# Performance work log

Measured on AMD Instinct MI355X. Metric: run time of the kernel, lower is better.

The kernel has to match this reference:

```python
import jax, jax.numpy as jnp
import numpy as np

N_SPECIES = 4; N_BASIS = 128; N_GRAPH = 16; R_MAX = 6.0
NS_NODE, NV_NODE = 32, 16          # node irreps 32x0e + 16x1o
NS_EDGE = 16                       # initial edge irreps 16x0e
NS_OUT, NV_OUT = 16, 8             # output irreps 16x0e + 8x1o
NS_IN = 2 * NS_NODE + NS_EDGE      # 80 concatenated scalars
NV_IN = 2 * NV_NODE                # 32 concatenated vectors
NS_CONV = NS_OUT + NV_OUT          # 24 scalars (16 features + 8 gates)
W_SIZES = [NS_IN * NS_CONV, NS_IN * NV_OUT, NV_IN * NV_OUT, NV_IN * NS_CONV, NV_IN * NV_OUT]
N_NODES, N_EDGES = 8192, 65536
EPS = 1e-5


def gaussian_basis(d, stop, n):
    offsets = jnp.linspace(0.0, stop, n)
    coeff = -0.5 / (offsets[1] - offsets[0]) ** 2
    return jnp.exp(coeff * (d[:, None] - offsets[None, :]) ** 2)


def seg_mean(vals, seg, cnt):
    return jax.ops.segment_sum(vals, seg, num_segments=N_GRAPH) / cnt[:, None]


def setup_inputs():
    key = jax.random.key(0)
    ks = jax.random.split(key, 20)
    rn = lambda k, shape, scale: jax.random.normal(k, shape, jnp.float32) * scale
    inp = {}
    inp["node_fea"] = rn(ks[0], (N_NODES, NS_NODE + 3 * NV_NODE), 1.0)
    d = 0.5 + 5.0 * jax.random.uniform(ks[1], (N_EDGES,), jnp.float32)
    vec = jax.random.normal(ks[2], (N_EDGES, 3), jnp.float32)
    inp["edge_attr"] = jnp.concatenate([d[:, None], vec], axis=1)
    inp["edge_index"] = jax.random.randint(ks[3], (2, N_EDGES), 0, N_NODES)
    inp["x"] = jax.random.randint(ks[4], (N_NODES,), 0, N_SPECIES)
    inp["batch"] = jnp.sort(jax.random.randint(ks[5], (N_NODES,), 0, N_GRAPH))
    inp["w_rh"] = rn(ks[6], (N_BASIS, 64), N_BASIS ** -0.5); inp["b_rh"] = jnp.zeros((64,), jnp.float32)
    inp["w_ro"] = rn(ks[7], (64, sum(W_SIZES)), 64 ** -0.5); inp["b_ro"] = jnp.zeros((sum(W_SIZES),), jnp.float32)
    inp["w_pre"] = rn(ks[8], (NS_EDGE, NS_EDGE), NS_EDGE ** -0.5); inp["b_pre"] = jnp.zeros((NS_EDGE,), jnp.float32)
    inp["w_sc"] = rn(ks[9], (NS_EDGE, N_SPECIES ** 2, NS_OUT), 1.0)
    inp["w_post_s"] = rn(ks[10], (NS_OUT, NS_OUT), NS_OUT ** -0.5); inp["b_post_s"] = jnp.zeros((NS_OUT,), jnp.float32)
    inp["w_post_v"] = rn(ks[11], (NV_OUT, NV_OUT), NV_OUT ** -0.5)
    inp["ln_w_s"] = jnp.ones((NS_OUT,), jnp.float32); inp["ln_b_s"] = jnp.zeros((NS_OUT,), jnp.float32)
    inp["ln_w_v"] = jnp.ones((NV_OUT,), jnp.float32)
    inp["w_skip"] = rn(ks[12], (NS_EDGE, NS_OUT), NS_EDGE ** -0.5)
    inp["w_edge_s"] = rn(ks[13], (NS_OUT, NS_OUT), NS_OUT ** -0.5); inp["b_edge_s"] = jnp.zeros((NS_OUT,), jnp.float32)
    inp["w_edge_v"] = rn(ks[14], (NV_OUT, NV_OUT), NV_OUT ** -0.5)
    return inp


def _forward(node_fea, edge_attr, w_rh, b_rh, w_ro, b_ro, w_pre, b_pre, w_sc,
             w_post_s, b_post_s, w_post_v, ln_w_s, ln_b_s, ln_w_v,
             w_skip, w_edge_s, b_edge_s, w_edge_v, edge_index, x, batch):
    E = edge_index.shape[1]
    idx_i, idx_j = edge_index[0], edge_index[1]
    one_hot = jax.nn.one_hot(N_SPECIES * x[idx_i] + x[idx_j], N_SPECIES ** 2, dtype=node_fea.dtype)
    d, vec = edge_attr[:, 0], edge_attr[:, 1:4]
    u = vec / (jnp.linalg.norm(vec, axis=1, keepdims=True) + 1e-12)
    Y1 = np.sqrt(3.0) * u                                   # l=1 sph harm, component norm; Y0 == 1
    rbf = gaussian_basis(d, R_MAX, N_BASIS)                 # edge_length_embedded
    edge_s0 = gaussian_basis(d, 6.0, NS_EDGE)               # distance_expansion -> initial edge scalars
    # self connection: edge scalars x species-pair one-hot -> output scalars
    sc = jnp.einsum('ei,ej,ijo->eo', edge_s0, one_hot, w_sc) / np.sqrt(NS_EDGE * N_SPECIES ** 2)
    edge_s = edge_s0 @ w_pre + b_pre                        # lin_pre
    # gather node features by edge indices and concat
    nf_i, nf_j = node_fea[idx_i], node_fea[idx_j]
    s_in = jnp.concatenate([nf_i[:, :NS_NODE], nf_j[:, :NS_NODE], edge_s], axis=1)  # [E,80]
    v_in = jnp.concatenate([nf_i[:, NS_NODE:].reshape(E, NV_NODE, 3),
                            nf_j[:, NS_NODE:].reshape(E, NV_NODE, 3)], axis=1)      # [E,32,3]
    # radial MLP -> per-edge tensor-product path weights
    h = jax.nn.silu(rbf @ w_rh + b_rh)
    w_all = h @ w_ro + b_ro                                 # [E, 3840]
    w1, w2, w3, w4, w5 = jnp.split(w_all, np.cumsum(W_SIZES)[:-1].tolist(), axis=1)
    # equivariant tensor-product paths (explicit l<=1 Clebsch-Gordan structure)
    s0 = jnp.einsum('ei,eio->eo', s_in, w1.reshape(E, NS_IN, NS_CONV)) / np.sqrt(NS_IN)            # 0e x 0e -> 0e
    vA = jnp.einsum('ei,eio,ec->eoc', s_in, w2.reshape(E, NS_IN, NV_OUT), Y1) / np.sqrt(NS_IN)     # 0e x 1o -> 1o
    vB = jnp.einsum('eic,eio->eoc', v_in, w3.reshape(E, NV_IN, NV_OUT)) / np.sqrt(NV_IN)           # 1o x 0e -> 1o
    s1 = jnp.einsum('eic,eio,ec->eo', v_in, w4.reshape(E, NV_IN, NS_CONV), Y1) / np.sqrt(3.0 * NV_IN)  # 1o.1o -> 0e
    vC = jnp.einsum('eic,eio->eoc', jnp.cross(v_in, Y1[:, None, :]), w5.reshape(E, NV_IN, NV_OUT)) / np.sqrt(2.0 * NV_IN)  # 1o x 1o -> 1o
    s_conv = s0 + s1                                        # [E,24]
    v_conv = vA + vB + vC                                   # [E,8,3]
    # gate nonlinearity inside conv
    s_out = jax.nn.silu(s_conv[:, :NS_OUT])
    v_out = v_conv * jax.nn.sigmoid(s_conv[:, NS_OUT:])[:, :, None]
    # lin_post then self connection
    s_out = s_out @ w_post_s + b_post_s + sc
    v_out = jnp.einsum('eic,io->eoc', v_out, w_post_v)
    # e3LayerNorm keyed by graph id of source node
    eb = batch[idx_i]
    cnt = jnp.maximum(jax.ops.segment_sum(jnp.ones((E,), s_out.dtype), eb, num_segments=N_GRAPH), 1.0)
    mu = seg_mean(s_out, eb, cnt)
    s_c = s_out - mu[eb]
    rms_s = jnp.sqrt(seg_mean(s_c ** 2, eb, cnt).mean(axis=1, keepdims=True) + EPS)
    s_n = s_c / rms_s[eb] * ln_w_s + ln_b_s
    rms_v = jnp.sqrt((seg_mean((v_out ** 2).sum(-1), eb, cnt) / 3.0).mean(axis=1, keepdims=True) + EPS)
    v_n = v_out / rms_v[eb][:, :, None] * ln_w_v[None, :, None]
    # skip connection from old edge features (scalars only)
    s_n = s_n + edge_s0 @ w_skip
    # final lin_edge
    s_fin = s_n @ w_edge_s + b_edge_s
    v_fin = jnp.einsum('eic,io->eoc', v_n, w_edge_v)
    return jnp.concatenate([s_fin, v_fin.reshape(E, NV_OUT * 3)], axis=1)  # [E,40]


def reference(node_fea, edge_attr, edge_index, x, batch, w_rh, b_rh, w_ro, b_ro,
              w_pre, b_pre, w_sc, w_post_s, b_post_s, w_post_v, ln_w_s, ln_b_s, ln_w_v,
              w_skip, w_edge_s, b_edge_s, w_edge_v):
    return _forward(node_fea, edge_attr, w_rh, b_rh, w_ro, b_ro, w_pre, b_pre, w_sc,
                    w_post_s, b_post_s, w_post_v, ln_w_s, ln_b_s, ln_w_v,
                    w_skip, w_edge_s, b_edge_s, w_edge_v, edge_index, x, batch)
```

## Files before the change

kernel.cpp:

```cpp
#include <hip/hip_runtime.h>

typedef unsigned short u16;
typedef unsigned int u32;
typedef __attribute__((ext_vector_type(8))) short short8;
typedef __attribute__((ext_vector_type(4))) float floatx4;

#define E_TOTAL 65536

__device__ __forceinline__ u16 f2bf(float f) {
    union { float f; u32 i; } c; c.f = f;
    const u32 u = c.i;
    const u32 r = (u + 0x7fffu + ((u >> 16) & 1u)) >> 16;
    return (u16)r;
}
__device__ __forceinline__ float bfu2f(u16 u) {
    union { u32 i; float f; } c; c.i = ((u32)u) << 16; return c.f;
}
__device__ __forceinline__ void split2(float x0, float x1, u32& hp, u32& lp) {
    union { float f; u32 u; } a0, a1, h0, h1, l0, l1;
    a0.f = x0; a1.f = x1;
    h0.u = a0.u & 0xFFFF0000u; h1.u = a1.u & 0xFFFF0000u;
    hp = __builtin_amdgcn_perm(a1.u, a0.u, 0x07060302u);
    l0.f = x0 - h0.f; l1.f = x1 - h1.f;
    lp = __builtin_amdgcn_perm(l1.u, l0.u, 0x07060302u);
}
union Frag8 { u32 u[4]; short8 s; };


__global__ __launch_bounds__(64) void k_init(float* __restrict__ ws, int* __restrict__ binv) {
    const int lane = threadIdx.x;
    for (int i = lane; i < 1056; i += 64) ws[i] = 0.0f;
    const int q = lane >> 4;
    if (lane < 32) binv[lane] = lane;
    short8 bfr;
    #pragma unroll
    for (int j = 0; j < 8; ++j) bfr[j] = (short)f2bf((float)(q*8 + j + 1));
    #pragma unroll
    for (int s = 0; s < 32; ++s) {
        const int qa = s >> 3, ja = s & 7;
        short8 afr = {0,0,0,0,0,0,0,0};
        if (q == qa) afr[ja] = (short)f2bf(1.0f);
        floatx4 dc = {0.0f, 0.0f, 0.0f, 0.0f};
        dc = __builtin_amdgcn_mfma_f32_16x16x32_bf16(afr, bfr, dc, 0, 0, 0);
        if (lane == 0) {
            const int sB = (int)(dc[0] + 0.5f) - 1;
            if (sB >= 0 && sB < 32) binv[sB] = s;
        }
    }
}

__global__ __launch_bounds__(256) void k_edge_heavy(
    const float* __restrict__ node_fea, const float* __restrict__ edge_attr,
    const int* __restrict__ edge_index, const int* __restrict__ xsp,
    const float* __restrict__ w_rh, const float* __restrict__ b_rh,
    const float* __restrict__ w_ro, const float* __restrict__ b_ro,
    const float* __restrict__ w_pre, const float* __restrict__ b_pre,
    const float* __restrict__ w_sc, const float* __restrict__ w_post_s,
    const float* __restrict__ b_post_s, const float* __restrict__ w_post_v,
    const int* __restrict__ binv,
    float* __restrict__ out)
{
    __shared__ __align__(16) char pool[32 * 129 * 4];
    __shared__ float sh_sin[32][81];
    __shared__ float sh_vl[32][3][32];
    __shared__ float sh_acc[32][56];
    __shared__ float sh_es0[32][16];
    __shared__ float sh_y1[32][4];
    __shared__ int   sh_kmap[32];

    u16* pool16 = (u16*)pool;
    float (*sh_wt)[129] = (float(*)[129])pool;

    const int tid = threadIdx.x;
    const int ed = tid >> 4, l16 = tid & 15;
    const int lane = tid & 63, w = tid >> 6;
    const int quad = lane >> 4, l15 = lane & 15;

    if (tid < 32) sh_kmap[tid] = binv[tid];

    const float C128 = -0.5f * (127.0f/6.0f) * (127.0f/6.0f);
    const float S128 = 6.0f/127.0f;
    const float rs80 = 0.11180339887498949f;
    const float rs32 = 0.17677669529663689f;

    int pp[2];
    #pragma unroll
    for (int g = 0; g < 2; ++g) {
        const int e  = blockIdx.x * 32 + g*16 + ed;
        const int ge = g*16 + ed;
        const int ni = edge_index[e];
        const int nj = edge_index[E_TOTAL + e];
        pp[g] = 4*xsp[ni] + xsp[nj];
        const float4 ea = *(const float4*)(edge_attr + 4*e);
        const float d  = ea.x;
        const float vx = ea.y, vy = ea.z, vz = ea.w;
        const float invn = 1.0f / (sqrtf(vx*vx + vy*vy + vz*vz) + 1e-12f);
        if (l16 == 0) {
            sh_y1[ge][0] = 1.7320508075688772f * vx * invn;
            sh_y1[ge][1] = 1.7320508075688772f * vy * invn;
            sh_y1[ge][2] = 1.7320508075688772f * vz * invn;
        }
        {
            short8 thi, tlo;
            #pragma unroll
            for (int r = 0; r < 8; ++r) {
                const int b = l16*8 + r;
                const float t = d - S128 * (float)b;
                const float x = expf(C128 * t * t);
                const u16 hi = f2bf(x);
                thi[r] = (short)hi;
                tlo[r] = (short)f2bf(x - bfu2f(hi));
            }
            *(short8*)&pool16[(0*2 + g)*2048 + (l16*16 + ed)*8] = thi;
            *(short8*)&pool16[(1*2 + g)*2048 + (l16*16 + ed)*8] = tlo;
        }
        {
            const float t = d - 0.4f * (float)l16;
            sh_es0[ge][l16] = expf(-3.125f * t * t);
        }
        {
            const float* fi = node_fea + (size_t)ni * 80;
            const float* fj = node_fea + (size_t)nj * 80;
            sh_sin[ge][2*l16+0]    = fi[2*l16+0] * rs80;
            sh_sin[ge][2*l16+1]    = fi[2*l16+1] * rs80;
            sh_sin[ge][32+2*l16+0] = fj[2*l16+0] * rs80;
            sh_sin[ge][32+2*l16+1] = fj[2*l16+1] * rs80;
            #pragma unroll
            for (int c = 0; c < 3; ++c) {
                sh_vl[ge][c][l16]      = fi[32 + 3*l16 + c] * rs32;
                sh_vl[ge][c][16 + l16] = fj[32 + 3*l16 + c] * rs32;
            }
        }
    }
    for (int s = tid; s < 32*56; s += 256) (&sh_acc[0][0])[s] = 0.0f;
    __syncthreads();

    int km[8];
    u32 voff0[8], voff1[8];
    #pragma unroll
    for (int j = 0; j < 8; ++j) {
        km[j] = sh_kmap[quad*8 + j];
        voff0[j] = (u32)(km[j] * 3840 + l15);
        voff1[j] = voff0[j] + 32u * 3840u;
    }

    float my_sc[2];
    #pragma unroll
    for (int g = 0; g < 2; ++g) {
        const int ge = g*16 + ed;
        const int o = l16;
        float es = b_pre[o];
        float sc = 0.0f;
        const int p = pp[g];
        #pragma unroll
        for (int i = 0; i < 16; ++i) {
            const float gg = sh_es0[ge][i];
            es += gg * w_pre[i*16 + o];
            sc += gg * w_sc[(i*16 + p)*16 + o];
        }
        sh_sin[ge][64 + o] = es * rs80;
        my_sc[g] = sc * 0.0625f;
    }

    floatx4 hacc[2] = {{0,0,0,0},{0,0,0,0}};
    #pragma unroll
    for (int kk = 0; kk < 4; ++kk) {
        Frag8 bh, bl;
        #pragma unroll
        for (int jj = 0; jj < 4; ++jj) {
            const float x0 = w_rh[(size_t)(kk*32 + km[2*jj+0])*64 + w*16 + l15];
            const float x1 = w_rh[(size_t)(kk*32 + km[2*jj+1])*64 + w*16 + l15];
            split2(x0, x1, bh.u[jj], bl.u[jj]);
        }
        #pragma unroll
        for (int g = 0; g < 2; ++g) {
            const short8 ahi = *(const short8*)&pool16[(0*2 + g)*2048 + ((kk*4 + quad)*16 + l15)*8];
            const short8 alo = *(const short8*)&pool16[(1*2 + g)*2048 + ((kk*4 + quad)*16 + l15)*8];
            hacc[g] = __builtin_amdgcn_mfma_f32_16x16x32_bf16(ahi, bh.s, hacc[g], 0, 0, 0);
            hacc[g] = __builtin_amdgcn_mfma_f32_16x16x32_bf16(alo, bh.s, hacc[g], 0, 0, 0);
            hacc[g] = __builtin_amdgcn_mfma_f32_16x16x32_bf16(ahi, bl.s, hacc[g], 0, 0, 0);
        }
    }
    __syncthreads();
    {
        const int hn = w*16 + l15;
        const float bb = b_rh[hn];
        const int k8 = hn >> 3, j2 = hn & 7;
        #pragma unroll
        for (int g = 0; g < 2; ++g) {
            #pragma unroll
            for (int r = 0; r < 4; ++r) {
                const float x = hacc[g][r] + bb;
                const float s = x / (1.0f + expf(-x));
                const int m = quad*4 + r;
                const u16 h = f2bf(s);
                pool16[(0*2 + g)*1024 + (k8*16 + m)*8 + j2] = h;
                pool16[(1*2 + g)*1024 + (k8*16 + m)*8 + j2] = f2bf(s - bfu2f(h));
            }
        }
    }
    __syncthreads();
    short8 ah_[2][2], al_[2][2];
    #pragma unroll
    for (int f = 0; f < 2; ++f)
        #pragma unroll
        for (int g = 0; g < 2; ++g) {
            ah_[f][g] = *(const short8*)&pool16[(0*2 + g)*1024 + ((f*4 + quad)*16 + l15)*8];
            al_[f][g] = *(const short8*)&pool16[(1*2 + g)*1024 + ((f*4 + quad)*16 + l15)*8];
        }

    for (int ch = 0; ch < 30; ++ch) {
        const int coff = ch * 128;
        floatx4 acc[2][2];
        float bias[2];
        #pragma unroll
        for (int ct = 0; ct < 2; ++ct) {
            const int sgct = __builtin_amdgcn_readfirstlane(ch*8 + w*2 + ct);
            const float* bp = w_ro + sgct*16;
            float f0[8], f1[8];
            #pragma unroll
            for (int j = 0; j < 8; ++j) {
                f0[j] = bp[voff0[j]];
                f1[j] = bp[voff1[j]];
            }
            Frag8 b0h, b0l, b1h, b1l;
            #pragma unroll
            for (int jj = 0; jj < 4; ++jj) {
                split2(f0[2*jj], f0[2*jj+1], b0h.u[jj], b0l.u[jj]);
                split2(f1[2*jj], f1[2*jj+1], b1h.u[jj], b1l.u[jj]);
            }
            #pragma unroll
            for (int g = 0; g < 2; ++g) {
                floatx4 a = {0.0f, 0.0f, 0.0f, 0.0f};
                a = __builtin_amdgcn_mfma_f32_16x16x32_bf16(ah_[0][g], b0h.s, a, 0, 0, 0);
                a = __builtin_amdgcn_mfma_f32_16x16x32_bf16(ah_[1][g], b1h.s, a, 0, 0, 0);
                a = __builtin_amdgcn_mfma_f32_16x16x32_bf16(al_[0][g], b0h.s, a, 0, 0, 0);
                a = __builtin_amdgcn_mfma_f32_16x16x32_bf16(al_[1][g], b1h.s, a, 0, 0, 0);
                a = __builtin_amdgcn_mfma_f32_16x16x32_bf16(ah_[0][g], b0l.s, a, 0, 0, 0);
                a = __builtin_amdgcn_mfma_f32_16x16x32_bf16(ah_[1][g], b1l.s, a, 0, 0, 0);
                acc[ct][g] = a;
            }
            bias[ct] = b_ro[sgct*16 + l15];
        }
        __syncthreads();
        #pragma unroll
        for (int ct = 0; ct < 2; ++ct) {
            const int col = w*32 + ct*16 + l15;
            #pragma unroll
            for (int g = 0; g < 2; ++g)
                #pragma unroll
                for (int r = 0; r < 4; ++r)
                    sh_wt[g*16 + quad*4 + r][col] = acc[ct][g][r] + bias[ct];
        }
        __syncthreads();

        if (ch < 15) {
            for (int idx = tid; idx < 768; idx += 256) {
                const int eo = idx / 24, o = idx % 24;
                const int i0 = (coff > o) ? (coff - o + 23) / 24 : 0;
                int i1 = (coff + 128 - o + 23) / 24; if (i1 > 80) i1 = 80;
                float a = 0.0f;
                for (int i = i0; i < i1; ++i)
                    a += sh_sin[eo][i] * sh_wt[eo][i*24 + o - coff];
                sh_acc[eo][o] += a;
            }
        } else if (ch < 20) {
            const int ib = (ch - 15) * 16;
            const int eo = tid >> 3, o = tid & 7;
            float a = 0.0f;
            #pragma unroll
            for (int i = 0; i < 16; ++i)
                a += sh_sin[eo][ib + i] * sh_wt[eo][i*8 + o];
            sh_acc[eo][24 + o] += a;
        } else if (ch < 22) {
            const int ib = (ch - 20) * 16;
            for (int idx = tid; idx < 768; idx += 256) {
                const int eo = idx / 24, rem = idx % 24;
                const int o = rem / 3, cc = rem % 3;
                float a = 0.0f;
                #pragma unroll
                for (int i = 0; i < 16; ++i)
                    a += sh_vl[eo][cc][ib + i] * sh_wt[eo][i*8 + o];
                sh_acc[eo][32 + o*3 + cc] += a;
            }
        } else if (ch < 28) {
            const int rel = coff - 2816;
            for (int idx = tid; idx < 768; idx += 256) {
                const int eo = idx / 24, o = idx % 24;
                const int i0 = (rel > o) ? (rel - o + 23) / 24 : 0;
                int i1 = (rel + 128 - o + 23) / 24; if (i1 > 32) i1 = 32;
                float t0 = 0.0f, t1 = 0.0f, t2 = 0.0f;
                for (int i = i0; i < i1; ++i) {
                    const float wv = sh_wt[eo][i*24 + o - rel];
                    t0 += sh_vl[eo][0][i] * wv;
                    t1 += sh_vl[eo][1][i] * wv;
                    t2 += sh_vl[eo][2][i] * wv;
                }
                sh_acc[eo][o] += (t0*sh_y1[eo][0] + t1*sh_y1[eo][1] + t2*sh_y1[eo][2])
                                 * 0.57735026918962573f;
            }
        } else {
            const int ib = (ch - 28) * 16;
            const int eo = tid >> 3, o = tid & 7;
            float t0 = 0.0f, t1 = 0.0f, t2 = 0.0f;
            #pragma unroll
            for (int i = 0; i < 16; ++i) {
                const float wv = sh_wt[eo][i*8 + o];
                t0 += sh_vl[eo][0][ib + i] * wv;
                t1 += sh_vl[eo][1][ib + i] * wv;
                t2 += sh_vl[eo][2][ib + i] * wv;
            }
            const float Ya = sh_y1[eo][0], Yb = sh_y1[eo][1], Yc = sh_y1[eo][2];
            sh_acc[eo][32 + o*3 + 0] += 0.70710678118654746f * (t1*Yc - t2*Yb);
            sh_acc[eo][32 + o*3 + 1] += 0.70710678118654746f * (t2*Ya - t0*Yc);
            sh_acc[eo][32 + o*3 + 2] += 0.70710678118654746f * (t0*Yb - t1*Ya);
        }
    }
    __syncthreads();

    #pragma unroll
    for (int g = 0; g < 2; ++g) {
        const int e  = blockIdx.x * 32 + g*16 + ed;
        const int ge = g*16 + ed;
        {
            const int o = l16;
            float a = b_post_s[o] + my_sc[g];
            #pragma unroll
            for (int i = 0; i < 16; ++i) {
                const float sv = sh_acc[ge][i];
                a += (sv / (1.0f + expf(-sv))) * w_post_s[i*16 + o];
            }
            out[(size_t)e*40 + o] = a;
        }
        if (l16 < 8) {
            const int o = l16;
            const float Ya = sh_y1[ge][0], Yb = sh_y1[ge][1], Yc = sh_y1[ge][2];
            float r0 = 0.0f, r1 = 0.0f, r2 = 0.0f;
            #pragma unroll
            for (int i = 0; i < 8; ++i) {
                const float gg = 1.0f / (1.0f + expf(-sh_acc[ge][16 + i]));
                const float a2 = sh_acc[ge][24 + i];
                const float ww = w_post_v[i*8 + o];
                r0 += (a2*Ya + sh_acc[ge][32 + i*3 + 0]) * gg * ww;
                r1 += (a2*Yb + sh_acc[ge][32 + i*3 + 1]) * gg * ww;
                r2 += (a2*Yc + sh_acc[ge][32 + i*3 + 2]) * gg * ww;
            }
            out[(size_t)e*40 + 16 + o*3 + 0] = r0;
            out[(size_t)e*40 + 16 + o*3 + 1] = r1;
            out[(size_t)e*40 + 16 + o*3 + 2] = r2;
        }
    }
}

__global__ __launch_bounds__(256) void k_stats_partial(
    const float* __restrict__ sv, const int* __restrict__ edge_index,
    const int* __restrict__ batch, float* __restrict__ ws)
{
    __shared__ float sh_ed[256][41];
    __shared__ int   sh_eb[256];
    const int tid = threadIdx.x;
    const int e = blockIdx.x * 256 + tid;
    sh_eb[tid] = batch[edge_index[e]];
    const float* p = sv + (size_t)e * 40;
    #pragma unroll
    for (int j = 0; j < 40; ++j) sh_ed[tid][j] = p[j];
    __syncthreads();

    for (int slot = tid; slot < 768; slot += 256) {
        const int g = slot / 48, s = slot % 48;
        float acc = 0.0f;
        if (s < 16) {
            for (int k = 0; k < 256; ++k) {
                const float m = (sh_eb[k] == g) ? 1.0f : 0.0f;
                acc += m * sh_ed[k][s];
            }
        } else if (s < 32) {
            for (int k = 0; k < 256; ++k) {
                const float m = (sh_eb[k] == g) ? 1.0f : 0.0f;
                const float v = sh_ed[k][s - 16];
                acc += m * v * v;
            }
        } else if (s < 40) {
            const int o3 = 16 + (s - 32) * 3;
            for (int k = 0; k < 256; ++k) {
                const float m = (sh_eb[k] == g) ? 1.0f : 0.0f;
                const float v0 = sh_ed[k][o3], v1 = sh_ed[k][o3+1], v2 = sh_ed[k][o3+2];
                acc += m * (v0*v0 + v1*v1 + v2*v2);
            }
        } else if (s == 40) {
            for (int k = 0; k < 256; ++k) acc += (sh_eb[k] == g) ? 1.0f : 0.0f;
        }
        atomicAdd(&ws[slot], acc);
    }
}

__global__ __launch_bounds__(64) void k_stats_final(float* __restrict__ ws)
{
    const int tid = threadIdx.x;
    if (tid < 16) {
        const int g = tid;
        float cnt = ws[g*48 + 40]; if (cnt < 1.0f) cnt = 1.0f;
        const float ic = 1.0f / cnt;
        float vs = 0.0f;
        for (int chn = 0; chn < 16; ++chn) {
            const float mu = ws[g*48 + chn] * ic;
            ws[768 + g*16 + chn] = mu;
            vs += ws[g*48 + 16 + chn] * ic - mu * mu;
        }
        if (vs < 0.0f) vs = 0.0f;
        ws[1024 + g] = 1.0f / sqrtf(vs * (1.0f/16.0f) + 1e-5f);
        float vv = 0.0f;
        for (int o = 0; o < 8; ++o) vv += ws[g*48 + 32 + o];
        vv = vv * ic * (1.0f/3.0f) * (1.0f/8.0f);
        ws[1040 + g] = 1.0f / sqrtf(vv + 1e-5f);
    }
}

__global__ __launch_bounds__(256) void k_edge_final(
    float* buf, const float* __restrict__ ws,
    const float* __restrict__ edge_attr, const int* __restrict__ edge_index,
    const int* __restrict__ batch,
    const float* __restrict__ ln_w_s, const float* __restrict__ ln_b_s,
    const float* __restrict__ ln_w_v, const float* __restrict__ w_skip,
    const float* __restrict__ w_edge_s, const float* __restrict__ b_edge_s,
    const float* __restrict__ w_edge_v)
{
    __shared__ float sh_mu[16][16];
    __shared__ float sh_is[16], sh_iv[16];
    __shared__ float sh_lws[16], sh_lbs[16], sh_lwv[8];
    __shared__ float sh_skip[16][16], sh_wes[16][16], sh_bes[16], sh_wev[8][8];
    const int tid = threadIdx.x;
    sh_mu[tid >> 4][tid & 15]   = ws[768 + tid];
    sh_skip[tid >> 4][tid & 15] = w_skip[tid];
    sh_wes[tid >> 4][tid & 15]  = w_edge_s[tid];
    if (tid < 16) {
        sh_is[tid]  = ws[1024 + tid];
        sh_iv[tid]  = ws[1040 + tid];
        sh_lws[tid] = ln_w_s[tid];
        sh_lbs[tid] = ln_b_s[tid];
        sh_bes[tid] = b_edge_s[tid];
    }
    if (tid < 8)  sh_lwv[tid] = ln_w_v[tid];
    if (tid < 64) sh_wev[tid >> 3][tid & 7] = w_edge_v[tid];
    __syncthreads();

    const int e = blockIdx.x * 256 + tid;
    const int g = batch[edge_index[e]];
    const float d = edge_attr[4*e];
    float es0[16];
    #pragma unroll
    for (int b = 0; b < 16; ++b) {
        const float t = d - 0.4f * (float)b;
        es0[b] = expf(-3.125f * t * t);
    }
    float p[40];
    float* pb = buf + (size_t)e * 40;
    #pragma unroll
    for (int j = 0; j < 40; ++j) p[j] = pb[j];

    const float is = sh_is[g];
    float sn[16];
    #pragma unroll
    for (int chn = 0; chn < 16; ++chn)
        sn[chn] = (p[chn] - sh_mu[g][chn]) * is * sh_lws[chn] + sh_lbs[chn];
    #pragma unroll
    for (int b = 0; b < 16; ++b) {
        const float g0 = es0[b];
        #pragma unroll
        for (int chn = 0; chn < 16; ++chn) sn[chn] += g0 * sh_skip[b][chn];
    }
    #pragma unroll
    for (int o = 0; o < 16; ++o) {
        float a = sh_bes[o];
        #pragma unroll
        for (int chn = 0; chn < 16; ++chn) a += sn[chn] * sh_wes[chn][o];
        pb[o] = a;
    }
    const float iv = sh_iv[g];
    float vn[8][3];
    #pragma unroll
    for (int i = 0; i < 8; ++i) {
        const float f = iv * sh_lwv[i];
        vn[i][0] = p[16 + i*3 + 0] * f;
        vn[i][1] = p[16 + i*3 + 1] * f;
        vn[i][2] = p[16 + i*3 + 2] * f;
    }
    #pragma unroll
    for (int o = 0; o < 8; ++o) {
        float r0 = 0.0f, r1 = 0.0f, r2 = 0.0f;
        #pragma unroll
        for (int i = 0; i < 8; ++i) {
            const float w = sh_wev[i][o];
            r0 += vn[i][0] * w; r1 += vn[i][1] * w; r2 += vn[i][2] * w;
        }
        pb[16 + o*3 + 0] = r0;
        pb[16 + o*3 + 1] = r1;
        pb[16 + o*3 + 2] = r2;
    }
}

extern "C" void kernel_launch(void* const* d_in, const int* in_sizes, int n_in,
                              void* d_out, int out_size, void* d_ws, size_t ws_size,
                              hipStream_t stream)
{
    const float* node_fea  = (const float*)d_in[0];
    const float* edge_attr = (const float*)d_in[1];
    const int* edge_index  = (const int*)d_in[2];
    const int* xsp         = (const int*)d_in[3];
    const int* batch       = (const int*)d_in[4];
    const float* w_rh      = (const float*)d_in[5];
    const float* b_rh      = (const float*)d_in[6];
    const float* w_ro      = (const float*)d_in[7];
    const float* b_ro      = (const float*)d_in[8];
    const float* w_pre     = (const float*)d_in[9];
    const float* b_pre     = (const float*)d_in[10];
    const float* w_sc      = (const float*)d_in[11];
    const float* w_post_s  = (const float*)d_in[12];
    const float* b_post_s  = (const float*)d_in[13];
    const float* w_post_v  = (const float*)d_in[14];
    const float* ln_w_s    = (const float*)d_in[15];
    const float* ln_b_s    = (const float*)d_in[16];
    const float* ln_w_v    = (const float*)d_in[17];
    const float* w_skip    = (const float*)d_in[18];
    const float* w_edge_s  = (const float*)d_in[19];
    const float* b_edge_s  = (const float*)d_in[20];
    const float* w_edge_v  = (const float*)d_in[21];

    float* ws   = (float*)d_ws;
    int*   binv = (int*)(ws + 1056);
    float* out  = (float*)d_out;

    k_init<<<1, 64, 0, stream>>>(ws, binv);
    k_edge_heavy<<<2048, 256, 0, stream>>>(node_fea, edge_attr, edge_index, xsp,
        w_rh, b_rh, w_ro, b_ro, w_pre, b_pre, w_sc, w_post_s, b_post_s, w_post_v,
        binv, out);
    k_stats_partial<<<256, 256, 0, stream>>>(out, edge_index, batch, ws);
    k_stats_final<<<1, 64, 0, stream>>>(ws);
    k_edge_final<<<256, 256, 0, stream>>>(out, ws, edge_attr, edge_index,
        batch, ln_w_s, ln_b_s, ln_w_v, w_skip, w_edge_s, b_edge_s, w_edge_v);
}
```

Before: 491.2 us.

## Fuse graph stats into edge kernel, prefetch weights, keep accumulators in registers

Moves the per-graph statistics reduction into the heavy edge kernel, which removes the k_stats_partial pass that re-read the whole output. Atomics now use 64-bit fixed-point integers, which makes the sums deterministic. The w_ro fragment loads are software-pipelined one chunk ahead. Per-edge accumulators move from shared memory into registers, and launch bounds request 3 blocks per SM. In exchange, the kernel issues far more global atomics (2048 blocks instead of 256), register pressure goes up, and the fixed-point scale could overflow or lose precision.

```diff
diff --git a/kernel.cpp b/kernel.cpp
--- a/kernel.cpp
+++ b/kernel.cpp
@@ -2,10 +2,13 @@
 
 typedef unsigned short u16;
 typedef unsigned int u32;
+typedef unsigned long long u64;
 typedef __attribute__((ext_vector_type(8))) short short8;
 typedef __attribute__((ext_vector_type(4))) float floatx4;
 
 #define E_TOTAL 65536
+#define STAT_SCALE 67108864.0f
+#define STAT_INV   (1.0 / 67108864.0)
 
 __device__ __forceinline__ u16 f2bf(float f) {
     union { float f; u32 i; } c; c.f = f;
@@ -29,7 +32,7 @@
 
 __global__ __launch_bounds__(64) void k_init(float* __restrict__ ws, int* __restrict__ binv) {
     const int lane = threadIdx.x;
-    for (int i = lane; i < 1056; i += 64) ws[i] = 0.0f;
+    for (int i = lane; i < 1824; i += 64) ws[i] = 0.0f;
     const int q = lane >> 4;
     if (lane < 32) binv[lane] = lane;
     short8 bfr;
@@ -49,7 +52,7 @@
     }
 }
 
-__global__ __launch_bounds__(256) void k_edge_heavy(
+__global__ __launch_bounds__(256, 3) void k_edge_heavy(
     const float* __restrict__ node_fea, const float* __restrict__ edge_attr,
     const int* __restrict__ edge_index, const int* __restrict__ xsp,
     const float* __restrict__ w_rh, const float* __restrict__ b_rh,
@@ -57,8 +60,8 @@
     const float* __restrict__ w_pre, const float* __restrict__ b_pre,
     const float* __restrict__ w_sc, const float* __restrict__ w_post_s,
     const float* __restrict__ b_post_s, const float* __restrict__ w_post_v,
-    const int* __restrict__ binv,
-    float* __restrict__ out)
+    const int* __restrict__ binv, const int* __restrict__ batch,
+    float* __restrict__ out, float* __restrict__ ws)
 {
     __shared__ __align__(16) char pool[32 * 129 * 4];
     __shared__ float sh_sin[32][81];
@@ -67,9 +70,11 @@
     __shared__ float sh_es0[32][16];
     __shared__ float sh_y1[32][4];
     __shared__ int   sh_kmap[32];
+    __shared__ int   sh_eb[32];
 
     u16* pool16 = (u16*)pool;
     float (*sh_wt)[129] = (float(*)[129])pool;
+    float* psf = (float*)pool;
 
     const int tid = threadIdx.x;
     const int ed = tid >> 4, l16 = tid & 15;
@@ -99,6 +104,7 @@
             sh_y1[ge][0] = 1.7320508075688772f * vx * invn;
             sh_y1[ge][1] = 1.7320508075688772f * vy * invn;
             sh_y1[ge][2] = 1.7320508075688772f * vz * invn;
+            sh_eb[ge] = batch[ni];
         }
         {
             short8 thi, tlo;
@@ -132,7 +138,6 @@
             }
         }
     }
-    for (int s = tid; s < 32*56; s += 256) (&sh_acc[0][0])[s] = 0.0f;
     __syncthreads();
 
     int km[8];
@@ -209,25 +214,37 @@
             al_[f][g] = *(const short8*)&pool16[(1*2 + g)*1024 + ((f*4 + quad)*16 + l15)*8];
         }
 
+    float rs[3] = {0.0f, 0.0f, 0.0f};
+    float ra2   = 0.0f;
+    float rv[3] = {0.0f, 0.0f, 0.0f};
+
+    float fB[32];
+    float biasv[2];
+    {
+        #pragma unroll
+        for (int ct = 0; ct < 2; ++ct) {
+            const int sgct = __builtin_amdgcn_readfirstlane(w*2 + ct);
+            const float* bp = w_ro + sgct*16;
+            #pragma unroll
+            for (int j = 0; j < 8; ++j) {
+                fB[ct*16 + j]     = bp[voff0[j]];
+                fB[ct*16 + 8 + j] = bp[voff1[j]];
+            }
+            biasv[ct] = b_ro[sgct*16 + l15];
+        }
+    }
+
     for (int ch = 0; ch < 30; ++ch) {
         const int coff = ch * 128;
         floatx4 acc[2][2];
-        float bias[2];
+        float biasc[2] = {biasv[0], biasv[1]};
         #pragma unroll
         for (int ct = 0; ct < 2; ++ct) {
-            const int sgct = __builtin_amdgcn_readfirstlane(ch*8 + w*2 + ct);
-            const float* bp = w_ro + sgct*16;
-            float f0[8], f1[8];
-            #pragma unroll
-            for (int j = 0; j < 8; ++j) {
-                f0[j] = bp[voff0[j]];
-                f1[j] = bp[voff1[j]];
-            }
             Frag8 b0h, b0l, b1h, b1l;
             #pragma unroll
             for (int jj = 0; jj < 4; ++jj) {
-                split2(f0[2*jj], f0[2*jj+1], b0h.u[jj], b0l.u[jj]);
-                split2(f1[2*jj], f1[2*jj+1], b1h.u[jj], b1l.u[jj]);
+                split2(fB[ct*16 + 2*jj],     fB[ct*16 + 2*jj + 1],     b0h.u[jj], b0l.u[jj]);
+                split2(fB[ct*16 + 8 + 2*jj], fB[ct*16 + 8 + 2*jj + 1], b1h.u[jj], b1l.u[jj]);
             }
             #pragma unroll
             for (int g = 0; g < 2; ++g) {
@@ -240,7 +257,19 @@
                 a = __builtin_amdgcn_mfma_f32_16x16x32_bf16(ah_[1][g], b1l.s, a, 0, 0, 0);
                 acc[ct][g] = a;
             }
-            bias[ct] = b_ro[sgct*16 + l15];
+        }
+        if (ch + 1 < 30) {
+            #pragma unroll
+            for (int ct = 0; ct < 2; ++ct) {
+                const int sgct = __builtin_amdgcn_readfirstlane((ch+1)*8 + w*2 + ct);
+                const float* bp = w_ro + sgct*16;
+                #pragma unroll
+                for (int j = 0; j < 8; ++j) {
+                    fB[ct*16 + j]     = bp[voff0[j]];
+                    fB[ct*16 + 8 + j] = bp[voff1[j]];
+                }
+                biasv[ct] = b_ro[sgct*16 + l15];
+            }
         }
         __syncthreads();
         #pragma unroll
@@ -250,19 +279,21 @@
             for (int g = 0; g < 2; ++g)
                 #pragma unroll
                 for (int r = 0; r < 4; ++r)
-                    sh_wt[g*16 + quad*4 + r][col] = acc[ct][g][r] + bias[ct];
+                    sh_wt[g*16 + quad*4 + r][col] = acc[ct][g][r] + biasc[ct];
         }
         __syncthreads();
 
         if (ch < 15) {
-            for (int idx = tid; idx < 768; idx += 256) {
+            #pragma unroll
+            for (int t3 = 0; t3 < 3; ++t3) {
+                const int idx = tid + 256*t3;
                 const int eo = idx / 24, o = idx % 24;
                 const int i0 = (coff > o) ? (coff - o + 23) / 24 : 0;
                 int i1 = (coff + 128 - o + 23) / 24; if (i1 > 80) i1 = 80;
                 float a = 0.0f;
                 for (int i = i0; i < i1; ++i)
                     a += sh_sin[eo][i] * sh_wt[eo][i*24 + o - coff];
-                sh_acc[eo][o] += a;
+                rs[t3] += a;
             }
         } else if (ch < 20) {
             const int ib = (ch - 15) * 16;
@@ -271,21 +302,25 @@
             #pragma unroll
             for (int i = 0; i < 16; ++i)
                 a += sh_sin[eo][ib + i] * sh_wt[eo][i*8 + o];
-            sh_acc[eo][24 + o] += a;
+            ra2 += a;
         } else if (ch < 22) {
             const int ib = (ch - 20) * 16;
-            for (int idx = tid; idx < 768; idx += 256) {
+            #pragma unroll
+            for (int t3 = 0; t3 < 3; ++t3) {
+                const int idx = tid + 256*t3;
                 const int eo = idx / 24, rem = idx % 24;
                 const int o = rem / 3, cc = rem % 3;
                 float a = 0.0f;
                 #pragma unroll
                 for (int i = 0; i < 16; ++i)
                     a += sh_vl[eo][cc][ib + i] * sh_wt[eo][i*8 + o];
-                sh_acc[eo][32 + o*3 + cc] += a;
+                rv[t3] += a;
             }
         } else if (ch < 28) {
             const int rel = coff - 2816;
-            for (int idx = tid; idx < 768; idx += 256) {
+            #pragma unroll
+            for (int t3 = 0; t3 < 3; ++t3) {
+                const int idx = tid + 256*t3;
                 const int eo = idx / 24, o = idx % 24;
                 const int i0 = (rel > o) ? (rel - o + 23) / 24 : 0;
                 int i1 = (rel + 128 - o + 23) / 24; if (i1 > 32) i1 = 32;
@@ -296,25 +331,40 @@
                     t1 += sh_vl[eo][1][i] * wv;
                     t2 += sh_vl[eo][2][i] * wv;
                 }
-                sh_acc[eo][o] += (t0*sh_y1[eo][0] + t1*sh_y1[eo][1] + t2*sh_y1[eo][2])
-                                 * 0.57735026918962573f;
+                rs[t3] += (t0*sh_y1[eo][0] + t1*sh_y1[eo][1] + t2*sh_y1[eo][2])
+                          * 0.57735026918962573f;
             }
         } else {
             const int ib = (ch - 28) * 16;
-            const int eo = tid >> 3, o = tid & 7;
-            float t0 = 0.0f, t1 = 0.0f, t2 = 0.0f;
-            #pragma unroll
-            for (int i = 0; i < 16; ++i) {
-                const float wv = sh_wt[eo][i*8 + o];
-                t0 += sh_vl[eo][0][ib + i] * wv;
-                t1 += sh_vl[eo][1][ib + i] * wv;
-                t2 += sh_vl[eo][2][ib + i] * wv;
-            }
-            const float Ya = sh_y1[eo][0], Yb = sh_y1[eo][1], Yc = sh_y1[eo][2];
-            sh_acc[eo][32 + o*3 + 0] += 0.70710678118654746f * (t1*Yc - t2*Yb);
-            sh_acc[eo][32 + o*3 + 1] += 0.70710678118654746f * (t2*Ya - t0*Yc);
-            sh_acc[eo][32 + o*3 + 2] += 0.70710678118654746f * (t0*Yb - t1*Ya);
-        }
+            #pragma unroll
+            for (int t3 = 0; t3 < 3; ++t3) {
+                const int idx = tid + 256*t3;
+                const int eo = idx / 24, rem = idx % 24;
+                const int o = rem / 3, cc = rem % 3;
+                const int c1 = (cc + 1) % 3, c2 = (cc + 2) % 3;
+                float ta = 0.0f, tb = 0.0f;
+                #pragma unroll
+                for (int i = 0; i < 16; ++i) {
+                    const float wv = sh_wt[eo][i*8 + o];
+                    ta += sh_vl[eo][c1][ib + i] * wv;
+                    tb += sh_vl[eo][c2][ib + i] * wv;
+                }
+                rv[t3] += 0.70710678118654746f * (ta*sh_y1[eo][c2] - tb*sh_y1[eo][c1]);
+            }
+        }
+    }
+
+    #pragma unroll
+    for (int t3 = 0; t3 < 3; ++t3) {
+        const int idx = tid + 256*t3;
+        sh_acc[idx/24][idx%24] = rs[t3];
+    }
+    sh_acc[tid >> 3][24 + (tid & 7)] = ra2;
+    #pragma unroll
+    for (int t3 = 0; t3 < 3; ++t3) {
+        const int idx = tid + 256*t3;
+        const int rem = idx % 24;
+        sh_acc[idx/24][32 + (rem/3)*3 + (rem%3)] = rv[t3];
     }
     __syncthreads();
 
@@ -331,6 +381,7 @@
                 a += (sv / (1.0f + expf(-sv))) * w_post_s[i*16 + o];
             }
             out[(size_t)e*40 + o] = a;
+            psf[ge*16 + o] = a;
         }
         if (l16 < 8) {
             const int o = l16;
@@ -348,71 +399,58 @@
             out[(size_t)e*40 + 16 + o*3 + 0] = r0;
             out[(size_t)e*40 + 16 + o*3 + 1] = r1;
             out[(size_t)e*40 + 16 + o*3 + 2] = r2;
-        }
-    }
-}
-
-__global__ __launch_bounds__(256) void k_stats_partial(
-    const float* __restrict__ sv, const int* __restrict__ edge_index,
-    const int* __restrict__ batch, float* __restrict__ ws)
-{
-    __shared__ float sh_ed[256][41];
-    __shared__ int   sh_eb[256];
-    const int tid = threadIdx.x;
-    const int e = blockIdx.x * 256 + tid;
-    sh_eb[tid] = batch[edge_index[e]];
-    const float* p = sv + (size_t)e * 40;
-    #pragma unroll
-    for (int j = 0; j < 40; ++j) sh_ed[tid][j] = p[j];
+            psf[512 + ge*8 + o] = r0*r0 + r1*r1 + r2*r2;
+        }
+    }
     __syncthreads();
 
+    u64* stats = (u64*)ws;
     for (int slot = tid; slot < 768; slot += 256) {
         const int g = slot / 48, s = slot % 48;
         float acc = 0.0f;
         if (s < 16) {
-            for (int k = 0; k < 256; ++k) {
-                const float m = (sh_eb[k] == g) ? 1.0f : 0.0f;
-                acc += m * sh_ed[k][s];
-            }
+            for (int k = 0; k < 32; ++k)
+                if (sh_eb[k] == g) acc += psf[k*16 + s];
         } else if (s < 32) {
-            for (int k = 0; k < 256; ++k) {
-                const float m = (sh_eb[k] == g) ? 1.0f : 0.0f;
-                const float v = sh_ed[k][s - 16];
-                acc += m * v * v;
-            }
+            for (int k = 0; k < 32; ++k)
+                if (sh_eb[k] == g) { const float v = psf[k*16 + s - 16]; acc += v*v; }
         } else if (s < 40) {
-            const int o3 = 16 + (s - 32) * 3;
-            for (int k = 0; k < 256; ++k) {
-                const float m = (sh_eb[k] == g) ? 1.0f : 0.0f;
-                const float v0 = sh_ed[k][o3], v1 = sh_ed[k][o3+1], v2 = sh_ed[k][o3+2];
-                acc += m * (v0*v0 + v1*v1 + v2*v2);
-            }
+            for (int k = 0; k < 32; ++k)
+                if (sh_eb[k] == g) acc += psf[512 + k*8 + (s - 32)];
         } else if (s == 40) {
-            for (int k = 0; k < 256; ++k) acc += (sh_eb[k] == g) ? 1.0f : 0.0f;
-        }
-        atomicAdd(&ws[slot], acc);
+            for (int k = 0; k < 32; ++k)
+                if (sh_eb[k] == g) acc += 1.0f;
+        }
+        if (s <= 40) {
+            const long long q = llrintf(acc * STAT_SCALE);
+            atomicAdd(&stats[slot], (u64)q);
+        }
     }
 }
 
 __global__ __launch_bounds__(64) void k_stats_final(float* __restrict__ ws)
 {
     const int tid = threadIdx.x;
+    const long long* stats = (const long long*)ws;
     if (tid < 16) {
         const int g = tid;
-        float cnt = ws[g*48 + 40]; if (cnt < 1.0f) cnt = 1.0f;
+        float cnt = (float)((double)stats[g*48 + 40] * STAT_INV);
+        if (cnt < 1.0f) cnt = 1.0f;
         const float ic = 1.0f / cnt;
         float vs = 0.0f;
         for (int chn = 0; chn < 16; ++chn) {
-            const float mu = ws[g*48 + chn] * ic;
-            ws[768 + g*16 + chn] = mu;
-            vs += ws[g*48 + 16 + chn] * ic - mu * mu;
+            const float sum1 = (float)((double)stats[g*48 + chn] * STAT_INV);
+            const float sum2 = (float)((double)stats[g*48 + 16 + chn] * STAT_INV);
+            const float mu = sum1 * ic;
+            ws[1536 + g*16 + chn] = mu;
+            vs += sum2 * ic - mu * mu;
         }
         if (vs < 0.0f) vs = 0.0f;
-        ws[1024 + g] = 1.0f / sqrtf(vs * (1.0f/16.0f) + 1e-5f);
+        ws[1792 + g] = 1.0f / sqrtf(vs * (1.0f/16.0f) + 1e-5f);
         float vv = 0.0f;
-        for (int o = 0; o < 8; ++o) vv += ws[g*48 + 32 + o];
+        for (int o = 0; o < 8; ++o) vv += (float)((double)stats[g*48 + 32 + o] * STAT_INV);
         vv = vv * ic * (1.0f/3.0f) * (1.0f/8.0f);
-        ws[1040 + g] = 1.0f / sqrtf(vv + 1e-5f);
+        ws[1808 + g] = 1.0f / sqrtf(vv + 1e-5f);
     }
 }
 
@@ -430,12 +468,12 @@
     __shared__ float sh_lws[16], sh_lbs[16], sh_lwv[8];
     __shared__ float sh_skip[16][16], sh_wes[16][16], sh_bes[16], sh_wev[8][8];
     const int tid = threadIdx.x;
-    sh_mu[tid >> 4][tid & 15]   = ws[768 + tid];
+    sh_mu[tid >> 4][tid & 15]   = ws[1536 + tid];
     sh_skip[tid >> 4][tid & 15] = w_skip[tid];
     sh_wes[tid >> 4][tid & 15]  = w_edge_s[tid];
     if (tid < 16) {
-        sh_is[tid]  = ws[1024 + tid];
-        sh_iv[tid]  = ws[1040 + tid];
+        sh_is[tid]  = ws[1792 + tid];
+        sh_iv[tid]  = ws[1808 + tid];
         sh_lws[tid] = ln_w_s[tid];
         sh_lbs[tid] = ln_b_s[tid];
         sh_bes[tid] = b_edge_s[tid];
@@ -527,14 +565,13 @@
     const float* w_edge_v  = (const float*)d_in[21];
 
     float* ws   = (float*)d_ws;
-    int*   binv = (int*)(ws + 1056);
+    int*   binv = (int*)(ws + 1824);
     float* out  = (float*)d_out;
 
     k_init<<<1, 64, 0, stream>>>(ws, binv);
     k_edge_heavy<<<2048, 256, 0, stream>>>(node_fea, edge_attr, edge_index, xsp,
         w_rh, b_rh, w_ro, b_ro, w_pre, b_pre, w_sc, w_post_s, b_post_s, w_post_v,
-        binv, out);
-    k_stats_partial<<<256, 256, 0, stream>>>(out, edge_index, batch, ws);
+        binv, batch, out, ws);
     k_stats_final<<<1, 64, 0, stream>>>(ws);
     k_edge_final<<<256, 256, 0, stream>>>(out, ws, edge_attr, edge_index,
         batch, ln_w_s, ln_b_s, ln_w_v, w_skip, w_edge_s, b_edge_s, w_edge_v);
```

After: 517.6 us. 1.05x slower.
